# Kernel tuning notes

Measured on AMD Instinct MI355X. Metric: run time of the kernel, lower is better.

Reference implementation:

```python
import jax, jax.numpy as jnp
import numpy as np

N_NODES = 50000
N_EDGES = 1600000
NODE_DIM = 64
EDGE_DIM = 32
HIDDEN = 128
OUT = 64


def setup_inputs() -> dict:
    key = jax.random.key(0)
    k1, k2, k3, k4, k5, k6, k7 = jax.random.split(key, 7)
    edge_index = jax.random.randint(k1, (2, N_EDGES), 0, N_NODES, dtype=jnp.int64 if jax.config.jax_enable_x64 else jnp.int32)
    node_features = jax.random.normal(k2, (N_NODES, NODE_DIM), dtype=jnp.float32)
    edge_features = jax.random.normal(k3, (N_EDGES, EDGE_DIM), dtype=jnp.float32)
    in_dim = EDGE_DIM + 2 * NODE_DIM
    # torch nn.Linear init scale ~ 1/sqrt(fan_in)
    W1 = jax.random.uniform(k4, (HIDDEN, in_dim), jnp.float32, -1.0, 1.0) / np.sqrt(in_dim)
    b1 = jax.random.uniform(k5, (HIDDEN,), jnp.float32, -1.0, 1.0) / np.sqrt(in_dim)
    W2 = jax.random.uniform(k6, (OUT, HIDDEN), jnp.float32, -1.0, 1.0) / np.sqrt(HIDDEN)
    b2 = jax.random.uniform(k7, (OUT,), jnp.float32, -1.0, 1.0) / np.sqrt(HIDDEN)
    return {"edge_index": edge_index, "node_features": node_features,
            "edge_features": edge_features, "W1": W1, "b1": b1, "W2": W2, "b2": b2}


def reference(edge_index, node_features, edge_features, W1, b1, W2, b2):
    src = node_features[edge_index[0]]  # [E, node_dim]
    tgt = node_features[edge_index[1]]  # [E, node_dim]
    x = jnp.concatenate([edge_features, src, tgt], axis=1)  # [E, edge_dim + 2*node_dim]
    h = jax.nn.relu(x @ W1.T + b1)  # [E, hidden]
    return h @ W2.T + b2  # [E, out]
```

## Files before the change

kernel.cpp:

```cpp
#include <hip/hip_runtime.h>

typedef __bf16 bf16x4 __attribute__((ext_vector_type(4)));
typedef __bf16 bf16x8 __attribute__((ext_vector_type(8)));
typedef float  f32x4  __attribute__((ext_vector_type(4)));

#define XS 168
#define HS 136
#define XPLANE (64 * XS * 2)
#define HPLANE (64 * HS * 2)

__device__ inline f32x4 mfma16(bf16x8 a, bf16x8 b, f32x4 c) {
  return __builtin_amdgcn_mfma_f32_16x16x32_bf16(a, b, c, 0, 0, 0);
}

struct bf2 { __bf16 h, l; };
__device__ inline bf2 split(float x) {
  bf2 r;
  r.h = (__bf16)x;
  r.l = (__bf16)(x - (float)r.h);
  return r;
}

__global__ __launch_bounds__(256, 3) void edge_mlp(
    const int* __restrict__ eidx, const float* __restrict__ nf,
    const float* __restrict__ ef, const float* __restrict__ W1,
    const float* __restrict__ b1, const float* __restrict__ W2,
    const float* __restrict__ b2, float* __restrict__ out, int E)
{
  __shared__ __attribute__((aligned(16))) char smem[2 * XPLANE];
  __bf16* const sXh = (__bf16*)smem;
  __bf16* const sXl = (__bf16*)(smem + XPLANE);
  __bf16* const sHh = (__bf16*)smem;
  __bf16* const sHl = (__bf16*)(smem + HPLANE);

  const int tid  = threadIdx.x;
  const int lane = tid & 63;
  const int wv   = tid >> 6;
  const int l16  = lane & 15;
  const int q    = lane >> 4;

  bf16x8 w1h[2][5], w1l[2][5];
#pragma unroll
  for (int jt = 0; jt < 2; ++jt) {
    const int j = 32 * wv + 16 * jt + l16;
#pragma unroll
    for (int kc = 0; kc < 5; ++kc) {
      const float* p = W1 + j * 160 + kc * 32 + q * 8;
#pragma unroll
      for (int i = 0; i < 8; ++i) {
        bf2 s = split(p[i]);
        w1h[jt][kc][i] = s.h;
        w1l[jt][kc][i] = s.l;
      }
    }
  }
  bf16x8 w2h[4], w2l[4];
  {
    const int o = 16 * wv + l16;
#pragma unroll
    for (int kc = 0; kc < 4; ++kc) {
      const float* p = W2 + o * 128 + kc * 32 + q * 8;
#pragma unroll
      for (int i = 0; i < 8; ++i) {
        bf2 s = split(p[i]);
        w2h[kc][i] = s.h;
        w2l[kc][i] = s.l;
      }
    }
  }
  float b1v[2][4], b2v[4];
#pragma unroll
  for (int jt = 0; jt < 2; ++jt)
#pragma unroll
    for (int r = 0; r < 4; ++r) b1v[jt][r] = b1[32 * wv + 16 * jt + 4 * q + r];
#pragma unroll
  for (int r = 0; r < 4; ++r) b2v[r] = b2[16 * wv + 4 * q + r];

  const float4* ef4 = (const float4*)ef;
  const float4* nf4 = (const float4*)nf;

  const int eL = tid >> 2;
  const int qq = tid & 3;
  const int ntiles = (E + 63) >> 6;

  float4 g[10];
  auto gather = [&](int tile_) {
    int e = tile_ * 64 + eL;
    if (e >= E) e = E - 1;
    const int s = eidx[e];
    const int t = eidx[E + e];
#pragma unroll
    for (int i = 0; i < 10; ++i) {
      const int fi = qq + 4 * i;
      const float4* p = (i < 2) ? (ef4 + e * 8 + fi)
                      : (i < 6) ? (nf4 + s * 16 + (fi - 8))
                                : (nf4 + t * 16 + (fi - 24));
      g[i] = *p;
    }
  };

  int tile = blockIdx.x;
  if (tile < ntiles) gather(tile);

  for (; tile < ntiles; tile += gridDim.x) {
    const int e0 = tile << 6;

    __syncthreads();

#pragma unroll
    for (int i = 0; i < 10; ++i) {
      const int fi = qq + 4 * i;
      const float4 v = g[i];
      bf16x4 hv, lv;
      { bf2 s0 = split(v.x); hv[0] = s0.h; lv[0] = s0.l; }
      { bf2 s1 = split(v.y); hv[1] = s1.h; lv[1] = s1.l; }
      { bf2 s2 = split(v.z); hv[2] = s2.h; lv[2] = s2.l; }
      { bf2 s3 = split(v.w); hv[3] = s3.h; lv[3] = s3.l; }
      *(bf16x4*)&sXh[eL * XS + fi * 4] = hv;
      *(bf16x4*)&sXl[eL * XS + fi * 4] = lv;
    }
    __syncthreads();

    {
      const int nxt = tile + gridDim.x;
      if (nxt < ntiles) gather(nxt);
    }

    f32x4 acc1[2][4];
#pragma unroll
    for (int jt = 0; jt < 2; ++jt)
#pragma unroll
      for (int et = 0; et < 4; ++et) acc1[jt][et] = (f32x4){0.f, 0.f, 0.f, 0.f};

#pragma unroll
    for (int kc = 0; kc < 5; ++kc) {
#pragma unroll
      for (int ep = 0; ep < 4; ep += 2) {
        bf16x8 xh[2], xl[2];
#pragma unroll
        for (int m = 0; m < 2; ++m) {
          const int off = (16 * (ep + m) + l16) * XS + kc * 32 + q * 8;
          xh[m] = *(const bf16x8*)&sXh[off];
          xl[m] = *(const bf16x8*)&sXl[off];
        }
#pragma unroll
        for (int m = 0; m < 2; ++m)
#pragma unroll
          for (int jt = 0; jt < 2; ++jt)
            acc1[jt][ep + m] = mfma16(w1h[jt][kc], xh[m], acc1[jt][ep + m]);
#pragma unroll
        for (int m = 0; m < 2; ++m)
#pragma unroll
          for (int jt = 0; jt < 2; ++jt)
            acc1[jt][ep + m] = mfma16(w1h[jt][kc], xl[m], acc1[jt][ep + m]);
#pragma unroll
        for (int m = 0; m < 2; ++m)
#pragma unroll
          for (int jt = 0; jt < 2; ++jt)
            acc1[jt][ep + m] = mfma16(w1l[jt][kc], xh[m], acc1[jt][ep + m]);
      }
    }

    __syncthreads();

#pragma unroll
    for (int jt = 0; jt < 2; ++jt) {
#pragma unroll
      for (int et = 0; et < 4; ++et) {
        bf16x4 hh, hl;
#pragma unroll
        for (int r = 0; r < 4; ++r) {
          const float h = fmaxf(acc1[jt][et][r] + b1v[jt][r], 0.f);
          bf2 s = split(h);
          hh[r] = s.h; hl[r] = s.l;
        }
        const int base = (16 * et + l16) * HS + 32 * wv + 16 * jt + 4 * q;
        *(bf16x4*)&sHh[base] = hh;
        *(bf16x4*)&sHl[base] = hl;
      }
    }
    __syncthreads();

    f32x4 acc2[4];
#pragma unroll
    for (int et = 0; et < 4; ++et) acc2[et] = (f32x4){0.f, 0.f, 0.f, 0.f};

#pragma unroll
    for (int kc = 0; kc < 4; ++kc) {
      bf16x8 hh[4], hl[4];
#pragma unroll
      for (int et = 0; et < 4; ++et) {
        const int off = (16 * et + l16) * HS + kc * 32 + q * 8;
        hh[et] = *(const bf16x8*)&sHh[off];
        hl[et] = *(const bf16x8*)&sHl[off];
      }
#pragma unroll
      for (int et = 0; et < 4; ++et) acc2[et] = mfma16(w2h[kc], hh[et], acc2[et]);
#pragma unroll
      for (int et = 0; et < 4; ++et) acc2[et] = mfma16(w2h[kc], hl[et], acc2[et]);
#pragma unroll
      for (int et = 0; et < 4; ++et) acc2[et] = mfma16(w2l[kc], hh[et], acc2[et]);
    }

#pragma unroll
    for (int et = 0; et < 4; ++et) {
      const int e = e0 + 16 * et + l16;
      if (e < E) {
        f32x4 o;
#pragma unroll
        for (int r = 0; r < 4; ++r) o[r] = acc2[et][r] + b2v[r];
        *(f32x4*)&out[e * 64 + 16 * wv + 4 * q] = o;
      }
    }
  }
}

extern "C" void kernel_launch(void* const* d_in, const int* in_sizes, int n_in,
                              void* d_out, int out_size, void* d_ws, size_t ws_size,
                              hipStream_t stream) {
  const int*   eidx = (const int*)d_in[0];
  const float* nf   = (const float*)d_in[1];
  const float* ef   = (const float*)d_in[2];
  const float* W1   = (const float*)d_in[3];
  const float* b1   = (const float*)d_in[4];
  const float* W2   = (const float*)d_in[5];
  const float* b2   = (const float*)d_in[6];
  float* out = (float*)d_out;
  const int E = in_sizes[0] / 2;

  dim3 grid(1536), block(256);
  hipLaunchKernelGGL(edge_mlp, grid, block, 0, stream,
                     eidx, nf, ef, W1, b1, W2, b2, out, E);
}
```

Measured before the change: 894.2 us.

## Split work across 8 waves per block and reload W2 per tile

Doubles the block to 512 threads (8 waves), so each wave owns 16 hidden units in layer 1 and a 16-output by 32-edge slice in layer 2. This halves the per-wave register-resident W1 fragments and the gather buffers. W2 is no longer held in registers but reloaded from global (L1/L2) and re-split to bf16 hi/lo every tile. The goal is lower register pressure and higher occupancy (launch bounds 512,4) to hide gather latency, at the cost of extra W2 loads and split arithmetic per tile.

```diff
diff --git a/kernel.cpp b/kernel.cpp
--- a/kernel.cpp
+++ b/kernel.cpp
@@ -21,7 +21,7 @@
   return r;
 }
 
-__global__ __launch_bounds__(256, 3) void edge_mlp(
+__global__ __launch_bounds__(512, 4) void edge_mlp(
     const int* __restrict__ eidx, const float* __restrict__ nf,
     const float* __restrict__ ef, const float* __restrict__ W1,
     const float* __restrict__ b1, const float* __restrict__ W2,
@@ -35,65 +35,51 @@
 
   const int tid  = threadIdx.x;
   const int lane = tid & 63;
-  const int wv   = tid >> 6;
+  const int w    = tid >> 6;
   const int l16  = lane & 15;
   const int q    = lane >> 4;
 
-  bf16x8 w1h[2][5], w1l[2][5];
-#pragma unroll
-  for (int jt = 0; jt < 2; ++jt) {
-    const int j = 32 * wv + 16 * jt + l16;
-#pragma unroll
-    for (int kc = 0; kc < 5; ++kc) {
-      const float* p = W1 + j * 160 + kc * 32 + q * 8;
-#pragma unroll
-      for (int i = 0; i < 8; ++i) {
-        bf2 s = split(p[i]);
-        w1h[jt][kc][i] = s.h;
-        w1l[jt][kc][i] = s.l;
-      }
-    }
+  bf16x8 w1h[5], w1l[5];
+#pragma unroll
+  for (int kc = 0; kc < 5; ++kc) {
+    const float4* p = (const float4*)(W1 + (16 * w + l16) * 160 + kc * 32 + q * 8);
+    const float4 a = p[0], b = p[1];
+    bf2 s;
+    s = split(a.x); w1h[kc][0] = s.h; w1l[kc][0] = s.l;
+    s = split(a.y); w1h[kc][1] = s.h; w1l[kc][1] = s.l;
+    s = split(a.z); w1h[kc][2] = s.h; w1l[kc][2] = s.l;
+    s = split(a.w); w1h[kc][3] = s.h; w1l[kc][3] = s.l;
+    s = split(b.x); w1h[kc][4] = s.h; w1l[kc][4] = s.l;
+    s = split(b.y); w1h[kc][5] = s.h; w1l[kc][5] = s.l;
+    s = split(b.z); w1h[kc][6] = s.h; w1l[kc][6] = s.l;
+    s = split(b.w); w1h[kc][7] = s.h; w1l[kc][7] = s.l;
   }
-  bf16x8 w2h[4], w2l[4];
-  {
-    const int o = 16 * wv + l16;
-#pragma unroll
-    for (int kc = 0; kc < 4; ++kc) {
-      const float* p = W2 + o * 128 + kc * 32 + q * 8;
-#pragma unroll
-      for (int i = 0; i < 8; ++i) {
-        bf2 s = split(p[i]);
-        w2h[kc][i] = s.h;
-        w2l[kc][i] = s.l;
-      }
-    }
-  }
-  float b1v[2][4], b2v[4];
-#pragma unroll
-  for (int jt = 0; jt < 2; ++jt)
-#pragma unroll
-    for (int r = 0; r < 4; ++r) b1v[jt][r] = b1[32 * wv + 16 * jt + 4 * q + r];
-#pragma unroll
-  for (int r = 0; r < 4; ++r) b2v[r] = b2[16 * wv + 4 * q + r];
+  float b1v[4], b2v[4];
+#pragma unroll
+  for (int r = 0; r < 4; ++r) b1v[r] = b1[16 * w + 4 * q + r];
+  const int os    = w & 3;
+  const int ebase = 32 * (w >> 2);
+#pragma unroll
+  for (int r = 0; r < 4; ++r) b2v[r] = b2[16 * os + 4 * q + r];
 
   const float4* ef4 = (const float4*)ef;
   const float4* nf4 = (const float4*)nf;
 
-  const int eL = tid >> 2;
-  const int qq = tid & 3;
+  const int eL = tid >> 3;
+  const int qq = tid & 7;
   const int ntiles = (E + 63) >> 6;
 
-  float4 g[10];
+  float4 g[5];
   auto gather = [&](int tile_) {
     int e = tile_ * 64 + eL;
     if (e >= E) e = E - 1;
     const int s = eidx[e];
     const int t = eidx[E + e];
 #pragma unroll
-    for (int i = 0; i < 10; ++i) {
-      const int fi = qq + 4 * i;
-      const float4* p = (i < 2) ? (ef4 + e * 8 + fi)
-                      : (i < 6) ? (nf4 + s * 16 + (fi - 8))
+    for (int i = 0; i < 5; ++i) {
+      const int fi = qq + 8 * i;
+      const float4* p = (i < 1) ? (ef4 + e * 8 + qq)
+                      : (i < 3) ? (nf4 + s * 16 + (fi - 8))
                                 : (nf4 + t * 16 + (fi - 24));
       g[i] = *p;
     }
@@ -108,8 +94,8 @@
     __syncthreads();
 
 #pragma unroll
-    for (int i = 0; i < 10; ++i) {
-      const int fi = qq + 4 * i;
+    for (int i = 0; i < 5; ++i) {
+      const int fi = qq + 8 * i;
       const float4 v = g[i];
       bf16x4 hv, lv;
       { bf2 s0 = split(v.x); hv[0] = s0.h; lv[0] = s0.l; }
@@ -126,11 +112,9 @@
       if (nxt < ntiles) gather(nxt);
     }
 
-    f32x4 acc1[2][4];
-#pragma unroll
-    for (int jt = 0; jt < 2; ++jt)
-#pragma unroll
-      for (int et = 0; et < 4; ++et) acc1[jt][et] = (f32x4){0.f, 0.f, 0.f, 0.f};
+    f32x4 acc1[4];
+#pragma unroll
+    for (int et = 0; et < 4; ++et) acc1[et] = (f32x4){0.f, 0.f, 0.f, 0.f};
 
 #pragma unroll
     for (int kc = 0; kc < 5; ++kc) {
@@ -145,71 +129,73 @@
         }
 #pragma unroll
         for (int m = 0; m < 2; ++m)
-#pragma unroll
-          for (int jt = 0; jt < 2; ++jt)
-            acc1[jt][ep + m] = mfma16(w1h[jt][kc], xh[m], acc1[jt][ep + m]);
+          acc1[ep + m] = mfma16(w1h[kc], xh[m], acc1[ep + m]);
 #pragma unroll
         for (int m = 0; m < 2; ++m)
-#pragma unroll
-          for (int jt = 0; jt < 2; ++jt)
-            acc1[jt][ep + m] = mfma16(w1h[jt][kc], xl[m], acc1[jt][ep + m]);
+          acc1[ep + m] = mfma16(w1h[kc], xl[m], acc1[ep + m]);
 #pragma unroll
         for (int m = 0; m < 2; ++m)
-#pragma unroll
-          for (int jt = 0; jt < 2; ++jt)
-            acc1[jt][ep + m] = mfma16(w1l[jt][kc], xh[m], acc1[jt][ep + m]);
-      }
-    }
-
-    __syncthreads();
-
-#pragma unroll
-    for (int jt = 0; jt < 2; ++jt) {
-#pragma unroll
-      for (int et = 0; et < 4; ++et) {
-        bf16x4 hh, hl;
-#pragma unroll
-        for (int r = 0; r < 4; ++r) {
-          const float h = fmaxf(acc1[jt][et][r] + b1v[jt][r], 0.f);
-          bf2 s = split(h);
-          hh[r] = s.h; hl[r] = s.l;
-        }
-        const int base = (16 * et + l16) * HS + 32 * wv + 16 * jt + 4 * q;
-        *(bf16x4*)&sHh[base] = hh;
-        *(bf16x4*)&sHl[base] = hl;
-      }
-    }
-    __syncthreads();
-
-    f32x4 acc2[4];
-#pragma unroll
-    for (int et = 0; et < 4; ++et) acc2[et] = (f32x4){0.f, 0.f, 0.f, 0.f};
+          acc1[ep + m] = mfma16(w1l[kc], xh[m], acc1[ep + m]);
+      }
+    }
+
+    __syncthreads();
+
+#pragma unroll
+    for (int et = 0; et < 4; ++et) {
+      bf16x4 hh, hl;
+#pragma unroll
+      for (int r = 0; r < 4; ++r) {
+        const float h = fmaxf(acc1[et][r] + b1v[r], 0.f);
+        bf2 s = split(h);
+        hh[r] = s.h; hl[r] = s.l;
+      }
+      const int base = (16 * et + l16) * HS + 16 * w + 4 * q;
+      *(bf16x4*)&sHh[base] = hh;
+      *(bf16x4*)&sHl[base] = hl;
+    }
+    __syncthreads();
+
+    f32x4 acc2[2];
+    acc2[0] = (f32x4){0.f, 0.f, 0.f, 0.f};
+    acc2[1] = (f32x4){0.f, 0.f, 0.f, 0.f};
 
 #pragma unroll
     for (int kc = 0; kc < 4; ++kc) {
-      bf16x8 hh[4], hl[4];
-#pragma unroll
-      for (int et = 0; et < 4; ++et) {
-        const int off = (16 * et + l16) * HS + kc * 32 + q * 8;
-        hh[et] = *(const bf16x8*)&sHh[off];
-        hl[et] = *(const bf16x8*)&sHl[off];
-      }
-#pragma unroll
-      for (int et = 0; et < 4; ++et) acc2[et] = mfma16(w2h[kc], hh[et], acc2[et]);
-#pragma unroll
-      for (int et = 0; et < 4; ++et) acc2[et] = mfma16(w2h[kc], hl[et], acc2[et]);
-#pragma unroll
-      for (int et = 0; et < 4; ++et) acc2[et] = mfma16(w2l[kc], hh[et], acc2[et]);
-    }
-
-#pragma unroll
-    for (int et = 0; et < 4; ++et) {
-      const int e = e0 + 16 * et + l16;
+      const float4* wp = (const float4*)(W2 + (16 * os + l16) * 128 + kc * 32 + q * 8);
+      asm volatile("" : "+v"(wp));
+      const float4 wa = wp[0], wb = wp[1];
+      bf16x8 w2h, w2l;
+      {
+        bf2 s;
+        s = split(wa.x); w2h[0] = s.h; w2l[0] = s.l;
+        s = split(wa.y); w2h[1] = s.h; w2l[1] = s.l;
+        s = split(wa.z); w2h[2] = s.h; w2l[2] = s.l;
+        s = split(wa.w); w2h[3] = s.h; w2l[3] = s.l;
+        s = split(wb.x); w2h[4] = s.h; w2l[4] = s.l;
+        s = split(wb.y); w2h[5] = s.h; w2l[5] = s.l;
+        s = split(wb.z); w2h[6] = s.h; w2l[6] = s.l;
+        s = split(wb.w); w2h[7] = s.h; w2l[7] = s.l;
+      }
+#pragma unroll
+      for (int eh = 0; eh < 2; ++eh) {
+        const int off = (ebase + 16 * eh + l16) * HS + kc * 32 + q * 8;
+        const bf16x8 hh = *(const bf16x8*)&sHh[off];
+        const bf16x8 hl = *(const bf16x8*)&sHl[off];
+        acc2[eh] = mfma16(w2h, hh, acc2[eh]);
+        acc2[eh] = mfma16(w2h, hl, acc2[eh]);
+        acc2[eh] = mfma16(w2l, hh, acc2[eh]);
+      }
+    }
+
+#pragma unroll
+    for (int eh = 0; eh < 2; ++eh) {
+      const int e = e0 + ebase + 16 * eh + l16;
       if (e < E) {
         f32x4 o;
 #pragma unroll
-        for (int r = 0; r < 4; ++r) o[r] = acc2[et][r] + b2v[r];
-        *(f32x4*)&out[e * 64 + 16 * wv + 4 * q] = o;
+        for (int r = 0; r < 4; ++r) o[r] = acc2[eh][r] + b2v[r];
+        *(f32x4*)&out[e * 64 + 16 * os + 4 * q] = o;
       }
     }
   }
@@ -228,7 +214,7 @@
   float* out = (float*)d_out;
   const int E = in_sizes[0] / 2;
 
-  dim3 grid(1536), block(256);
+  dim3 grid(1024), block(512);
   hipLaunchKernelGGL(edge_mlp, grid, block, 0, stream,
                      eidx, nf, ef, W1, b1, W2, b2, out, E);
 }
```

After: 811.8 us. 9.2% less time.
